# Performance work log

Measured on AMD Instinct MI355X. Metric: run time of the kernel, lower is better.

Reference implementation:

```python
import jax, jax.numpy as jnp
import numpy as np

N_T = 8
N_R = 2
NOISE = 1e-12  # 10**(-120/10)
B = 65536


def setup_inputs() -> dict:
    key = jax.random.key(0)
    ks = jax.random.split(key, 7)
    return {
        "theta1": jax.random.normal(ks[0], (B, 264), dtype=jnp.float32),
        "G1r": jax.random.normal(ks[1], (B, N_R, 100), dtype=jnp.float32),
        "G1i": jax.random.normal(ks[2], (B, N_R, 100), dtype=jnp.float32),
        "G2r": jax.random.normal(ks[3], (B, N_R, 100), dtype=jnp.float32),
        "G2i": jax.random.normal(ks[4], (B, N_R, 100), dtype=jnp.float32),
        "Ur": jax.random.normal(ks[5], (B, 100, N_T), dtype=jnp.float32),
        "Ui": jax.random.normal(ks[6], (B, 100, N_T), dtype=jnp.float32),
    }


def _rate(phi, Fsig, Fintf):
    # phi: [B, N_r, N_t], Fsig/Fintf: [B, N_t, N_r]
    A = jnp.einsum("bnt,btr->bnr", phi, Fsig)    # signal term  [B, N_r, N_r]
    C = jnp.einsum("bnt,btr->bnr", phi, Fintf)   # interference [B, N_r, N_r]
    # Mu = C C^H + noise (elementwise scalar add, faithful to torch source)
    Mu = jnp.einsum("bnr,bmr->bnm", C, jnp.conj(C)) + NOISE
    inner = jnp.einsum("brn,bnm,bms->brs", jnp.conj(A).transpose(0, 2, 1) if False else jnp.conj(jnp.swapaxes(A, 1, 2)), jnp.linalg.inv(Mu), A)
    # note: torch does 1 + matrix (elementwise), not identity add
    return jnp.real(jnp.log(jnp.linalg.det(1.0 + inner)))  # [B]


def reference(theta1, G1r, G1i, G2r, G2i, Ur, Ui):
    M1N1 = N_T * N_R  # 16
    F1 = theta1[:, 200:200 + M1N1] + 1j * theta1[:, 200 + M1N1:200 + 2 * M1N1]
    F2 = theta1[:, 200 + 2 * M1N1:200 + 3 * M1N1] + 1j * theta1[:, 200 + 3 * M1N1:]
    # power normalization: F * sqrt(2 / (F^H F))
    F1 = F1 * jnp.sqrt(2.0 / jnp.sum(jnp.conj(F1) * F1, axis=1, keepdims=True))
    F2 = F2 * jnp.sqrt(2.0 / jnp.sum(jnp.conj(F2) * F2, axis=1, keepdims=True))
    F1m = F1.reshape(-1, N_T, N_R)
    F2m = F2.reshape(-1, N_T, N_R)

    theta = theta1[:, 0:100] + 1j * theta1[:, 100:200]  # [B, 100]
    G1 = G1r + 1j * G1i
    G2 = G2r + 1j * G2i
    U = Ur + 1j * Ui

    # phi = G @ diag(theta) @ U, vectorized over batch
    phi1 = jnp.einsum("bnk,bk,bkt->bnt", G1, theta, U)  # [B, N_r, N_t]
    phi2 = jnp.einsum("bnk,bk,bkt->bnt", G2, theta, U)

    R1 = _rate(phi1, F1m, F2m)
    R2 = _rate(phi2, F2m, F1m)
    R = jnp.maximum(-R1, -R2)
    return jnp.sum(R) / theta1.shape[0]
```

## Files before the change

kernel.cpp:

```cpp
#include <hip/hip_runtime.h>
#include <math.h>

#define NOISE 1e-12f
#define WSZ 1064

__device__ __forceinline__ float2 cmul(float2 a, float2 b) {
    return make_float2(a.x*b.x - a.y*b.y, a.x*b.y + a.y*b.x);
}
__device__ __forceinline__ float2 cconjmul(float2 a, float2 b) {
    return make_float2(a.x*b.x + a.y*b.y, a.x*b.y - a.y*b.x);
}
__device__ __forceinline__ float2 cmulconj(float2 a, float2 b) {
    return make_float2(a.x*b.x + a.y*b.y, a.y*b.x - a.x*b.y);
}
__device__ __forceinline__ float2 cadd(float2 a, float2 b){ return make_float2(a.x+b.x, a.y+b.y); }
__device__ __forceinline__ float2 csub(float2 a, float2 b){ return make_float2(a.x-b.x, a.y-b.y); }
__device__ __forceinline__ float2 cscale(float s, float2 a){ return make_float2(s*a.x, s*a.y); }

__global__ __launch_bounds__(256) void rate_kernel(
    const float* __restrict__ t1,
    const float* __restrict__ G1r, const float* __restrict__ G1i,
    const float* __restrict__ G2r, const float* __restrict__ G2i,
    const float* __restrict__ Ur,  const float* __restrict__ Ui,
    float* __restrict__ partial)
{
    __shared__ float lds[4 * WSZ];
    __shared__ float2 ent[4][4][16];
    __shared__ float wsum[4];
    const int wave = threadIdx.x >> 6;
    const int lane = threadIdx.x & 63;
    const int t  = lane & 7;
    const int k0 = lane >> 3;
    const int e8 = k0;
    const int nn = (e8 >> 1) & 1;
    const int rr = e8 & 1;
    float* W = lds + wave * WSZ;

    for (int it = 0; it < 4; ++it) {
        const long b = (long)blockIdx.x * 16 + (long)wave * 4 + it;
        const float* tb   = t1  + b * 264;
        const float* g1rb = G1r + b * 200;
        const float* g1ib = G1i + b * 200;
        const float* g2rb = G2r + b * 200;
        const float* g2ib = G2i + b * 200;
        const float* urb  = Ur  + b * 800;
        const float* uib  = Ui  + b * 800;

        asm volatile("s_waitcnt lgkmcnt(0)" ::: "memory");
        __builtin_amdgcn_wave_barrier();
        if (lane < 25) {
            float4 r = ((const float4*)tb)[lane];
            float4 i = ((const float4*)(tb + 100))[lane];
            float2* d = (float2*)W + lane * 4;
            d[0] = make_float2(r.x, i.x);
            d[1] = make_float2(r.y, i.y);
            d[2] = make_float2(r.z, i.z);
            d[3] = make_float2(r.w, i.w);
        }
        if (lane < 50) {
            float4 r = ((const float4*)g1rb)[lane];
            float4 i = ((const float4*)g1ib)[lane];
            float2* d = (float2*)(W + 200) + lane * 4;
            d[0] = make_float2(r.x, i.x);
            d[1] = make_float2(r.y, i.y);
            d[2] = make_float2(r.z, i.z);
            d[3] = make_float2(r.w, i.w);
            r = ((const float4*)g2rb)[lane];
            i = ((const float4*)g2ib)[lane];
            d = (float2*)(W + 600) + lane * 4;
            d[0] = make_float2(r.x, i.x);
            d[1] = make_float2(r.y, i.y);
            d[2] = make_float2(r.z, i.z);
            d[3] = make_float2(r.w, i.w);
        }
        if (lane < 16)
            ((float4*)(W + 1000))[lane] = ((const float4*)(tb + 200))[lane];
        asm volatile("s_waitcnt lgkmcnt(0)" ::: "memory");
        __builtin_amdgcn_wave_barrier();

        float p[8] = {0,0,0,0,0,0,0,0};

        #define LDU(s) make_float2(urb[(s)*64 + lane], uib[(s)*64 + lane])
        #define CBODY(k, u) {                                        \
            float2 th = *(const float2*)(W + 2*(k));                 \
            float2 a  = *(const float2*)(W + 200 + 2*(k));           \
            float2 c  = *(const float2*)(W + 400 + 2*(k));           \
            float2 d2 = *(const float2*)(W + 600 + 2*(k));           \
            float2 e2 = *(const float2*)(W + 800 + 2*(k));           \
            float wr = th.x*(u).x - th.y*(u).y;                      \
            float wi = th.x*(u).y + th.y*(u).x;                      \
            p[0] += a.x*wr  - a.y*wi;   p[1] += a.x*wi  + a.y*wr;    \
            p[2] += c.x*wr  - c.y*wi;   p[3] += c.x*wi  + c.y*wr;    \
            p[4] += d2.x*wr - d2.y*wi;  p[5] += d2.x*wi + d2.y*wr;   \
            p[6] += e2.x*wr - e2.y*wi;  p[7] += e2.x*wi + e2.y*wr; }

        float2 u0 = LDU(0), u1 = LDU(1), u2 = LDU(2), u3 = LDU(3);
        const int ctail = 768 + (lane < 32 ? lane : 31);
        #pragma unroll 1
        for (int g = 0; g < 3; ++g) {
            const int s = 4 * g;
            float2 n0, n1, n2, n3;
            if (g < 2) {
                n0 = LDU(s + 4); n1 = LDU(s + 5);
                n2 = LDU(s + 6); n3 = LDU(s + 7);
            } else {
                n0 = make_float2(urb[ctail], uib[ctail]);
                n1 = n2 = n3 = n0;
            }
            CBODY(8*s + k0,      u0);
            CBODY(8*s + 8 + k0,  u1);
            CBODY(8*s + 16 + k0, u2);
            CBODY(8*s + 24 + k0, u3);
            u0 = n0; u1 = n1; u2 = n2; u3 = n3;
        }
        if (k0 < 4) {
            CBODY(96 + k0, u0);
        }
        #undef LDU
        #undef CBODY

        #pragma unroll
        for (int q = 0; q < 8; ++q) {
            p[q] += __shfl_xor(p[q], 8);
            p[q] += __shfl_xor(p[q], 32);
        }
        float4 ph;
        {
            float k0r = nn ? p[2] : p[0], s0r = nn ? p[0] : p[2];
            float k0i = nn ? p[3] : p[1], s0i = nn ? p[1] : p[3];
            float k1r = nn ? p[6] : p[4], s1r = nn ? p[4] : p[6];
            float k1i = nn ? p[7] : p[5], s1i = nn ? p[5] : p[7];
            ph.x = k0r + __shfl_xor(s0r, 16);
            ph.y = k0i + __shfl_xor(s0i, 16);
            ph.z = k1r + __shfl_xor(s1r, 16);
            ph.w = k1i + __shfl_xor(s1i, 16);
        }

        float s1, s2;
        {
            int idx = lane & 15;
            int sel = (lane >> 4) & 1;
            float fr = W[1000 + sel*32 + idx];
            float fi = W[1016 + sel*32 + idx];
            float m = fr*fr + fi*fi;
            #pragma unroll
            for (int s = 1; s < 16; s <<= 1) m += __shfl_xor(m, s);
            float other = __shfl_xor(m, 16);
            float nrm1 = sel ? other : m;
            float nrm2 = sel ? m : other;
            s1 = sqrtf(2.0f / nrm1);
            s2 = sqrtf(2.0f / nrm2);
        }

        {
            int jf = t*2 + rr;
            float2 f1 = make_float2(W[1000 + jf], W[1016 + jf]);
            float2 f2 = make_float2(W[1032 + jf], W[1048 + jf]);
            float2 phi1n = make_float2(ph.x, ph.y);
            float2 phi2n = make_float2(ph.z, ph.w);
            bool lo = (e8 < 4);
            float2 E0 = cmul(phi1n, lo ? f1 : f2);
            float2 E1 = cmul(phi2n, lo ? f2 : f1);
            #pragma unroll
            for (int s = 1; s < 8; s <<= 1) {
                E0.x += __shfl_xor(E0.x, s); E0.y += __shfl_xor(E0.y, s);
                E1.x += __shfl_xor(E1.x, s); E1.y += __shfl_xor(E1.y, s);
            }
            if (t == 0) {
                ent[wave][it][e8]     = cscale(lo ? s1 : s2, E0);
                ent[wave][it][e8 + 8] = cscale(lo ? s2 : s1, E1);
            }
        }
    }
    asm volatile("s_waitcnt lgkmcnt(0)" ::: "memory");
    __builtin_amdgcn_wave_barrier();

    float negR = 0.0f;
    if (lane < 8) {
        const float2* e = &ent[wave][lane >> 1][(lane & 1) * 8];
        float2 A00=e[0], A01=e[1], A10=e[2], A11=e[3];
        float2 C00=e[4], C01=e[5], C10=e[6], C11=e[7];
        float mu00 = C00.x*C00.x + C00.y*C00.y + C01.x*C01.x + C01.y*C01.y + NOISE;
        float mu11 = C10.x*C10.x + C10.y*C10.y + C11.x*C11.x + C11.y*C11.y + NOISE;
        float2 mu01 = cadd(cmulconj(C00, C10), cmulconj(C01, C11));
        mu01.x += NOISE;
        float det = mu00*mu11 - (mu01.x*mu01.x + mu01.y*mu01.y);
        float inv = 1.0f / det;
        float2 mu01c = make_float2(mu01.x, -mu01.y);
        float2 X00 = cscale(inv, csub(cscale(mu11, A00), cmul(mu01,  A10)));
        float2 X01 = cscale(inv, csub(cscale(mu11, A01), cmul(mu01,  A11)));
        float2 X10 = cscale(inv, csub(cscale(mu00, A10), cmul(mu01c, A00)));
        float2 X11 = cscale(inv, csub(cscale(mu00, A11), cmul(mu01c, A01)));
        float2 I00 = cadd(cconjmul(A00, X00), cconjmul(A10, X10));
        float2 I01 = cadd(cconjmul(A00, X01), cconjmul(A10, X11));
        float2 I10 = cadd(cconjmul(A01, X00), cconjmul(A11, X10));
        float2 I11 = cadd(cconjmul(A01, X01), cconjmul(A11, X11));
        I00.x += 1.0f; I01.x += 1.0f; I10.x += 1.0f; I11.x += 1.0f;
        float2 dT = csub(cmul(I00, I11), cmul(I01, I10));
        negR = -0.5f * logf(dT.x*dT.x + dT.y*dT.y);
    }
    float m = fmaxf(negR, __shfl_xor(negR, 1));
    m += __shfl_xor(m, 2);
    m += __shfl_xor(m, 4);
    if (lane == 0) wsum[wave] = m;

    __syncthreads();
    if (threadIdx.x == 0)
        partial[blockIdx.x] = (wsum[0] + wsum[1]) + (wsum[2] + wsum[3]);
}

__global__ __launch_bounds__(256) void reduce_kernel(
    const float* __restrict__ partial, int n, float invB, float* __restrict__ out)
{
    __shared__ float sd[256];
    float s = 0.0f;
    for (int i = threadIdx.x; i < n; i += 256) s += partial[i];
    sd[threadIdx.x] = s;
    __syncthreads();
    for (int o = 128; o > 0; o >>= 1) {
        if ((int)threadIdx.x < o) sd[threadIdx.x] += sd[threadIdx.x + o];
        __syncthreads();
    }
    if (threadIdx.x == 0) out[0] = sd[0] * invB;
}

extern "C" void kernel_launch(void* const* d_in, const int* in_sizes, int n_in,
                              void* d_out, int out_size, void* d_ws, size_t ws_size,
                              hipStream_t stream) {
    const float* t1  = (const float*)d_in[0];
    const float* G1r = (const float*)d_in[1];
    const float* G1i = (const float*)d_in[2];
    const float* G2r = (const float*)d_in[3];
    const float* G2i = (const float*)d_in[4];
    const float* Ur  = (const float*)d_in[5];
    const float* Ui  = (const float*)d_in[6];

    const int B = in_sizes[0] / 264;
    const int nblocks = B / 16;
    float* partial = (float*)d_ws;

    rate_kernel<<<nblocks, 256, 0, stream>>>(t1, G1r, G1i, G2r, G2i, Ur, Ui, partial);
    reduce_kernel<<<1, 256, 0, stream>>>(partial, nblocks, 1.0f / (float)B, (float*)d_out);
}
```

Before: 145.4 us.

## Prefetch next batch element's theta/G/F into registers during current compute

Software-pipelines the per-wave loop over four batch elements. The next element's theta, G1, G2 and F loads are issued into registers before the current element's compute, then written to LDS at the end of the iteration. This hides global load latency behind the phi accumulation and reductions, at the cost of extra live registers that may reduce occupancy.

```diff
diff --git a/kernel.cpp b/kernel.cpp
--- a/kernel.cpp
+++ b/kernel.cpp
@@ -36,47 +36,56 @@
     const int rr = e8 & 1;
     float* W = lds + wave * WSZ;
 
+    float4 sv_tr, sv_ti, sv_ar, sv_ai, sv_br, sv_bi, sv_f;
+    #define STAGE_LOAD(bb) {                                           \
+        const float* tb_  = t1  + (long)(bb) * 264;                    \
+        const float* g1r_ = G1r + (long)(bb) * 200;                    \
+        const float* g1i_ = G1i + (long)(bb) * 200;                    \
+        const float* g2r_ = G2r + (long)(bb) * 200;                    \
+        const float* g2i_ = G2i + (long)(bb) * 200;                    \
+        if (lane < 25) { sv_tr = ((const float4*)tb_)[lane];           \
+                         sv_ti = ((const float4*)(tb_ + 100))[lane]; } \
+        if (lane < 50) { sv_ar = ((const float4*)g1r_)[lane];          \
+                         sv_ai = ((const float4*)g1i_)[lane];          \
+                         sv_br = ((const float4*)g2r_)[lane];          \
+                         sv_bi = ((const float4*)g2i_)[lane]; }        \
+        if (lane < 16)   sv_f  = ((const float4*)(tb_ + 200))[lane];   \
+    }
+    #define STAGE_WRITE() {                                            \
+        if (lane < 25) {                                               \
+            float2* d = (float2*)W + lane * 4;                         \
+            d[0] = make_float2(sv_tr.x, sv_ti.x);                      \
+            d[1] = make_float2(sv_tr.y, sv_ti.y);                      \
+            d[2] = make_float2(sv_tr.z, sv_ti.z);                      \
+            d[3] = make_float2(sv_tr.w, sv_ti.w);                      \
+        }                                                              \
+        if (lane < 50) {                                               \
+            float2* d = (float2*)(W + 200) + lane * 4;                 \
+            d[0] = make_float2(sv_ar.x, sv_ai.x);                      \
+            d[1] = make_float2(sv_ar.y, sv_ai.y);                      \
+            d[2] = make_float2(sv_ar.z, sv_ai.z);                      \
+            d[3] = make_float2(sv_ar.w, sv_ai.w);                      \
+            d = (float2*)(W + 600) + lane * 4;                         \
+            d[0] = make_float2(sv_br.x, sv_bi.x);                      \
+            d[1] = make_float2(sv_br.y, sv_bi.y);                      \
+            d[2] = make_float2(sv_br.z, sv_bi.z);                      \
+            d[3] = make_float2(sv_br.w, sv_bi.w);                      \
+        }                                                              \
+        if (lane < 16) ((float4*)(W + 1000))[lane] = sv_f;             \
+    }
+
+    const long bbase = (long)blockIdx.x * 16 + (long)wave * 4;
+    STAGE_LOAD(bbase);
+    STAGE_WRITE();
+
     for (int it = 0; it < 4; ++it) {
-        const long b = (long)blockIdx.x * 16 + (long)wave * 4 + it;
-        const float* tb   = t1  + b * 264;
-        const float* g1rb = G1r + b * 200;
-        const float* g1ib = G1i + b * 200;
-        const float* g2rb = G2r + b * 200;
-        const float* g2ib = G2i + b * 200;
-        const float* urb  = Ur  + b * 800;
-        const float* uib  = Ui  + b * 800;
-
         asm volatile("s_waitcnt lgkmcnt(0)" ::: "memory");
         __builtin_amdgcn_wave_barrier();
-        if (lane < 25) {
-            float4 r = ((const float4*)tb)[lane];
-            float4 i = ((const float4*)(tb + 100))[lane];
-            float2* d = (float2*)W + lane * 4;
-            d[0] = make_float2(r.x, i.x);
-            d[1] = make_float2(r.y, i.y);
-            d[2] = make_float2(r.z, i.z);
-            d[3] = make_float2(r.w, i.w);
-        }
-        if (lane < 50) {
-            float4 r = ((const float4*)g1rb)[lane];
-            float4 i = ((const float4*)g1ib)[lane];
-            float2* d = (float2*)(W + 200) + lane * 4;
-            d[0] = make_float2(r.x, i.x);
-            d[1] = make_float2(r.y, i.y);
-            d[2] = make_float2(r.z, i.z);
-            d[3] = make_float2(r.w, i.w);
-            r = ((const float4*)g2rb)[lane];
-            i = ((const float4*)g2ib)[lane];
-            d = (float2*)(W + 600) + lane * 4;
-            d[0] = make_float2(r.x, i.x);
-            d[1] = make_float2(r.y, i.y);
-            d[2] = make_float2(r.z, i.z);
-            d[3] = make_float2(r.w, i.w);
-        }
-        if (lane < 16)
-            ((float4*)(W + 1000))[lane] = ((const float4*)(tb + 200))[lane];
-        asm volatile("s_waitcnt lgkmcnt(0)" ::: "memory");
-        __builtin_amdgcn_wave_barrier();
+
+        if (it < 3) STAGE_LOAD(bbase + it + 1);
+
+        const float* urb = Ur + (bbase + it) * 800;
+        const float* uib = Ui + (bbase + it) * 800;
 
         float p[8] = {0,0,0,0,0,0,0,0};
 
@@ -171,7 +180,15 @@
                 ent[wave][it][e8 + 8] = cscale(lo ? s2 : s1, E1);
             }
         }
-    }
+
+        if (it < 3) {
+            asm volatile("s_waitcnt lgkmcnt(0)" ::: "memory");
+            __builtin_amdgcn_wave_barrier();
+            STAGE_WRITE();
+        }
+    }
+    #undef STAGE_LOAD
+    #undef STAGE_WRITE
     asm volatile("s_waitcnt lgkmcnt(0)" ::: "memory");
     __builtin_amdgcn_wave_barrier();
 
```

Result: slower. 150.2 us (+3.3%).

## Double-buffer per-wave staging with direct global-to-LDS loads

Applied to the files above, without the earlier changes.

Replaces register-staged loads and interleaving stores with global_load_lds DMA straight into LDS, keeping the raw planar layout (real and imaginary arrays separate). The next batch element's theta/G/F data is prefetched into a second LDS buffer while the current one is computed, using vmcnt waits. This removes VGPR round-trips and lets loads overlap compute. In exchange it doubles LDS use per block, which may lower occupancy. The inner loop now needs two scalar LDS reads per complex value instead of one float2 read, and the vmcnt(6) count must exactly match the loads issued.

```diff
diff --git a/kernel.cpp b/kernel.cpp
--- a/kernel.cpp
+++ b/kernel.cpp
@@ -16,6 +16,12 @@
 __device__ __forceinline__ float2 cadd(float2 a, float2 b){ return make_float2(a.x+b.x, a.y+b.y); }
 __device__ __forceinline__ float2 csub(float2 a, float2 b){ return make_float2(a.x-b.x, a.y-b.y); }
 __device__ __forceinline__ float2 cscale(float s, float2 a){ return make_float2(s*a.x, s*a.y); }
+
+typedef const void __attribute__((address_space(1)))* gas_t;
+typedef void __attribute__((address_space(3)))* las_t;
+__device__ __forceinline__ void gll16(const float* g, float* l) {
+    __builtin_amdgcn_global_load_lds((gas_t)g, (las_t)l, 16, 0, 0);
+}
 
 __global__ __launch_bounds__(256) void rate_kernel(
     const float* __restrict__ t1,
@@ -24,7 +30,7 @@
     const float* __restrict__ Ur,  const float* __restrict__ Ui,
     float* __restrict__ partial)
 {
-    __shared__ float lds[4 * WSZ];
+    __shared__ float lds[4 * 2 * WSZ];
     __shared__ float2 ent[4][4][16];
     __shared__ float wsum[4];
     const int wave = threadIdx.x >> 6;
@@ -34,61 +40,48 @@
     const int e8 = k0;
     const int nn = (e8 >> 1) & 1;
     const int rr = e8 & 1;
-    float* W = lds + wave * WSZ;
+    float* Wbuf = lds + wave * 2 * WSZ;
+
+    #define STAGE(dst, bb) {                                                  \
+        const float* tb_ = t1 + (long)(bb) * 264;                             \
+        gll16(tb_ + lane * 4, (dst));                        \
+        if (lane < 2)  gll16(tb_ + 256 + lane * 4, (dst) + 256);              \
+        if (lane < 50) {                                                      \
+            gll16(G1r + (long)(bb) * 200 + lane * 4, (dst) + 264);            \
+            gll16(G1i + (long)(bb) * 200 + lane * 4, (dst) + 464);            \
+            gll16(G2r + (long)(bb) * 200 + lane * 4, (dst) + 664);            \
+            gll16(G2i + (long)(bb) * 200 + lane * 4, (dst) + 864);            \
+        }                                                                     \
+    }
+
+    const long bbase = (long)blockIdx.x * 16 + (long)wave * 4;
+    STAGE(Wbuf, bbase);
 
     for (int it = 0; it < 4; ++it) {
-        const long b = (long)blockIdx.x * 16 + (long)wave * 4 + it;
-        const float* tb   = t1  + b * 264;
-        const float* g1rb = G1r + b * 200;
-        const float* g1ib = G1i + b * 200;
-        const float* g2rb = G2r + b * 200;
-        const float* g2ib = G2i + b * 200;
-        const float* urb  = Ur  + b * 800;
-        const float* uib  = Ui  + b * 800;
-
-        asm volatile("s_waitcnt lgkmcnt(0)" ::: "memory");
-        __builtin_amdgcn_wave_barrier();
-        if (lane < 25) {
-            float4 r = ((const float4*)tb)[lane];
-            float4 i = ((const float4*)(tb + 100))[lane];
-            float2* d = (float2*)W + lane * 4;
-            d[0] = make_float2(r.x, i.x);
-            d[1] = make_float2(r.y, i.y);
-            d[2] = make_float2(r.z, i.z);
-            d[3] = make_float2(r.w, i.w);
-        }
-        if (lane < 50) {
-            float4 r = ((const float4*)g1rb)[lane];
-            float4 i = ((const float4*)g1ib)[lane];
-            float2* d = (float2*)(W + 200) + lane * 4;
-            d[0] = make_float2(r.x, i.x);
-            d[1] = make_float2(r.y, i.y);
-            d[2] = make_float2(r.z, i.z);
-            d[3] = make_float2(r.w, i.w);
-            r = ((const float4*)g2rb)[lane];
-            i = ((const float4*)g2ib)[lane];
-            d = (float2*)(W + 600) + lane * 4;
-            d[0] = make_float2(r.x, i.x);
-            d[1] = make_float2(r.y, i.y);
-            d[2] = make_float2(r.z, i.z);
-            d[3] = make_float2(r.w, i.w);
-        }
-        if (lane < 16)
-            ((float4*)(W + 1000))[lane] = ((const float4*)(tb + 200))[lane];
-        asm volatile("s_waitcnt lgkmcnt(0)" ::: "memory");
-        __builtin_amdgcn_wave_barrier();
+        float* W = Wbuf + (it & 1) * WSZ;
+
+        if (it < 3) {
+            STAGE(Wbuf + ((it + 1) & 1) * WSZ, bbase + it + 1);
+            asm volatile("s_waitcnt vmcnt(6)" ::: "memory");
+        } else {
+            asm volatile("s_waitcnt vmcnt(0)" ::: "memory");
+        }
+        __builtin_amdgcn_sched_barrier(0);
+
+        const float* urb = Ur + (bbase + it) * 800;
+        const float* uib = Ui + (bbase + it) * 800;
 
         float p[8] = {0,0,0,0,0,0,0,0};
 
         #define LDU(s) make_float2(urb[(s)*64 + lane], uib[(s)*64 + lane])
         #define CBODY(k, u) {                                        \
-            float2 th = *(const float2*)(W + 2*(k));                 \
-            float2 a  = *(const float2*)(W + 200 + 2*(k));           \
-            float2 c  = *(const float2*)(W + 400 + 2*(k));           \
-            float2 d2 = *(const float2*)(W + 600 + 2*(k));           \
-            float2 e2 = *(const float2*)(W + 800 + 2*(k));           \
-            float wr = th.x*(u).x - th.y*(u).y;                      \
-            float wi = th.x*(u).y + th.y*(u).x;                      \
+            float thr = W[(k)],      thi = W[100 + (k)];             \
+            float2 a  = make_float2(W[264 + (k)], W[464 + (k)]);     \
+            float2 c  = make_float2(W[364 + (k)], W[564 + (k)]);     \
+            float2 d2 = make_float2(W[664 + (k)], W[864 + (k)]);     \
+            float2 e2 = make_float2(W[764 + (k)], W[964 + (k)]);     \
+            float wr = thr*(u).x - thi*(u).y;                        \
+            float wi = thr*(u).y + thi*(u).x;                        \
             p[0] += a.x*wr  - a.y*wi;   p[1] += a.x*wi  + a.y*wr;    \
             p[2] += c.x*wr  - c.y*wi;   p[3] += c.x*wi  + c.y*wr;    \
             p[4] += d2.x*wr - d2.y*wi;  p[5] += d2.x*wi + d2.y*wr;   \
@@ -140,8 +133,8 @@
         {
             int idx = lane & 15;
             int sel = (lane >> 4) & 1;
-            float fr = W[1000 + sel*32 + idx];
-            float fi = W[1016 + sel*32 + idx];
+            float fr = W[200 + sel*32 + idx];
+            float fi = W[216 + sel*32 + idx];
             float m = fr*fr + fi*fi;
             #pragma unroll
             for (int s = 1; s < 16; s <<= 1) m += __shfl_xor(m, s);
@@ -154,8 +147,8 @@
 
         {
             int jf = t*2 + rr;
-            float2 f1 = make_float2(W[1000 + jf], W[1016 + jf]);
-            float2 f2 = make_float2(W[1032 + jf], W[1048 + jf]);
+            float2 f1 = make_float2(W[200 + jf], W[216 + jf]);
+            float2 f2 = make_float2(W[232 + jf], W[248 + jf]);
             float2 phi1n = make_float2(ph.x, ph.y);
             float2 phi2n = make_float2(ph.z, ph.w);
             bool lo = (e8 < 4);
@@ -172,6 +165,7 @@
             }
         }
     }
+    #undef STAGE
     asm volatile("s_waitcnt lgkmcnt(0)" ::: "memory");
     __builtin_amdgcn_wave_barrier();
 
```

Measured after the change: 144.8 us. No clear change (-0.4%).
